# Optimization experiments

Measured on AMD Instinct MI355X. Metric: run time of the kernel, lower is better.

Reference implementation:

```python
import jax, jax.numpy as jnp
import numpy as np

BN_EPS = 1e-5


def setup_inputs() -> dict:
    key = jax.random.key(0)
    k1, k2, k3, k4 = jax.random.split(key, 4)
    B, C, H, W = 16, 128, 128, 128
    x = jax.random.normal(k1, (B, C, H, W), dtype=jnp.float32)
    gamma = jax.random.normal(k2, (1,), dtype=jnp.float32)
    bn_weight = jax.random.uniform(k3, (C,), dtype=jnp.float32)
    bn_bias = jax.random.normal(k4, (C,), dtype=jnp.float32)
    return {"x": x, "gamma": gamma, "bn_weight": bn_weight, "bn_bias": bn_bias}


def reference(x, gamma, bn_weight, bn_bias):
    B, C, H, W = x.shape
    q = x.reshape(B, C, H * W)                      # proj_query: [B, C, HW]
    # energy[b, i, j] = <channel i, channel j>
    energy = jnp.einsum('bin,bjn->bij', q, q)       # [B, C, C]
    energy_new = jnp.max(energy, axis=-1, keepdims=True) - energy
    attention = jax.nn.softmax(energy_new, axis=-1)  # [B, C, C]
    out = jnp.einsum('bij,bjn->bin', attention, q)  # [B, C, HW]
    out = out.reshape(B, C, H, W)
    out = gamma * out
    # BatchNorm2d in training mode: batch statistics over (B, H, W) per channel
    mean = jnp.mean(out, axis=(0, 2, 3), keepdims=True)
    var = jnp.var(out, axis=(0, 2, 3), keepdims=True)  # biased variance
    out = (out - mean) * jax.lax.rsqrt(var + BN_EPS)
    out = out * bn_weight[None, :, None, None] + bn_bias[None, :, None, None]
    return out + x
```

## Files before the change

kernel.cpp:

```cpp
#include <hip/hip_runtime.h>

#define BB 16
#define CC 128
#define NN 16384
#define BN_EPS 1e-5f

typedef unsigned short u16;
typedef short short8 __attribute__((ext_vector_type(8)));
typedef float floatx4 __attribute__((ext_vector_type(4)));

__device__ inline float b2f(u16 u) {
    union { unsigned int i; float f; } c; c.i = ((unsigned int)u) << 16; return c.f;
}
__device__ inline u16 f2b(float f) {
    union { float f; unsigned int i; } c; c.f = f;
    unsigned int r = c.i + 0x7fffu + ((c.i >> 16) & 1u);
    return (u16)(r >> 16);
}

#define K1_LD 72
__global__ __launch_bounds__(256, 4) void k_gram(const float* __restrict__ x,
                                                 float* __restrict__ energy,
                                                 float* __restrict__ S)
{
    __shared__ u16 th[128 * K1_LD];
    __shared__ u16 tl[128 * K1_LD];
    const int b     = blockIdx.x >> 6;
    const int chunk = blockIdx.x & 63;
    const int k0    = chunk * 256;
    const int t     = threadIdx.x;
    const int w = t >> 6, lane = t & 63, quad = lane >> 4, colL = lane & 15;

    floatx4 acc[2][8];
#pragma unroll
    for (int rt = 0; rt < 2; ++rt)
#pragma unroll
        for (int ct = 0; ct < 8; ++ct) acc[rt][ct] = {0.f, 0.f, 0.f, 0.f};
    float rs[8];
#pragma unroll
    for (int it = 0; it < 8; ++it) rs[it] = 0.f;

    const float* xb = x + (size_t)b * CC * NN;
    const int rrow = t >> 4;
    const int c4   = t & 15;
    for (int s = 0; s < 4; ++s) {
        const int ks = k0 + s * 64;
        __syncthreads();
#pragma unroll
        for (int it = 0; it < 8; ++it) {
            int row = it * 16 + rrow;
            float4 v = *(const float4*)(xb + (size_t)row * NN + ks + c4 * 4);
            u16 h0 = f2b(v.x), h1 = f2b(v.y), h2 = f2b(v.z), h3 = f2b(v.w);
            uint2 hv, lv;
            hv.x = (unsigned)h0 | ((unsigned)h1 << 16);
            hv.y = (unsigned)h2 | ((unsigned)h3 << 16);
            lv.x = (unsigned)f2b(v.x - b2f(h0)) | ((unsigned)f2b(v.y - b2f(h1)) << 16);
            lv.y = (unsigned)f2b(v.z - b2f(h2)) | ((unsigned)f2b(v.w - b2f(h3)) << 16);
            *(uint2*)&th[row * K1_LD + c4 * 4] = hv;
            *(uint2*)&tl[row * K1_LD + c4 * 4] = lv;
            rs[it] += (v.x + v.y) + (v.z + v.w);
        }
        __syncthreads();
        const int rbase = w * 32;
#pragma unroll
        for (int ks2 = 0; ks2 < 2; ++ks2) {
            const int kk = ks2 * 32 + quad * 8;
            short8 a0h = *(const short8*)&th[(rbase + colL) * K1_LD + kk];
            short8 a1h = *(const short8*)&th[(rbase + 16 + colL) * K1_LD + kk];
            short8 a0l = *(const short8*)&tl[(rbase + colL) * K1_LD + kk];
            short8 a1l = *(const short8*)&tl[(rbase + 16 + colL) * K1_LD + kk];
#pragma unroll
            for (int ct = 0; ct < 8; ++ct) {
                short8 bh = *(const short8*)&th[(ct * 16 + colL) * K1_LD + kk];
                short8 bl = *(const short8*)&tl[(ct * 16 + colL) * K1_LD + kk];
                acc[0][ct] = __builtin_amdgcn_mfma_f32_16x16x32_bf16(a0h, bh, acc[0][ct], 0, 0, 0);
                acc[1][ct] = __builtin_amdgcn_mfma_f32_16x16x32_bf16(a1h, bh, acc[1][ct], 0, 0, 0);
                acc[0][ct] = __builtin_amdgcn_mfma_f32_16x16x32_bf16(a0l, bh, acc[0][ct], 0, 0, 0);
                acc[1][ct] = __builtin_amdgcn_mfma_f32_16x16x32_bf16(a1l, bh, acc[1][ct], 0, 0, 0);
                acc[0][ct] = __builtin_amdgcn_mfma_f32_16x16x32_bf16(a0h, bl, acc[0][ct], 0, 0, 0);
                acc[1][ct] = __builtin_amdgcn_mfma_f32_16x16x32_bf16(a1h, bl, acc[1][ct], 0, 0, 0);
            }
        }
    }
    float* eb = energy + b * CC * CC;
#pragma unroll
    for (int rt = 0; rt < 2; ++rt)
#pragma unroll
        for (int ct = 0; ct < 8; ++ct)
#pragma unroll
            for (int r = 0; r < 4; ++r) {
                int row = w * 32 + rt * 16 + quad * 4 + r;
                int col = ct * 16 + colL;
                atomicAdd(&eb[row * CC + col], acc[rt][ct][r]);
            }
#pragma unroll
    for (int it = 0; it < 8; ++it) {
        float ps = rs[it];
#pragma unroll
        for (int off = 8; off > 0; off >>= 1) ps += __shfl_down(ps, off, 16);
        if (colL == 0) atomicAdd(&S[b * CC + it * 16 + w * 4 + quad], ps);
    }
}

__global__ __launch_bounds__(256) void k_soft(const float* __restrict__ energy,
                                              const float* __restrict__ S,
                                              u16* __restrict__ attb,
                                              float* __restrict__ meanacc,
                                              float* __restrict__ e2acc)
{
    const int b = blockIdx.x >> 7;
    const int i = blockIdx.x & 127;
    const int t = threadIdx.x;
    __shared__ float att[128];
    __shared__ float red[256];
    const float* E = energy + b * CC * CC;

    float e = (t < 128) ? E[i * CC + t] : 3.0e38f;
    red[t] = e; __syncthreads();
    for (int s2 = 128; s2 > 0; s2 >>= 1) { if (t < s2) red[t] = fminf(red[t], red[t + s2]); __syncthreads(); }
    float emin = red[0]; __syncthreads();

    float a = (t < 128) ? expf(emin - e) : 0.f;
    red[t] = a; __syncthreads();
    for (int s2 = 128; s2 > 0; s2 >>= 1) { if (t < s2) red[t] += red[t + s2]; __syncthreads(); }
    float Z = red[0]; __syncthreads();

    float attf = 0.f;
    if (t < 128) {
        u16 ab = f2b(a / Z);
        attf = b2f(ab);
        attb[((size_t)b * CC + i) * CC + t] = ab;
        att[t] = attf;
    }
    float mp = (t < 128) ? attf * S[b * CC + t] : 0.f;
    red[t] = mp; __syncthreads();
    for (int s2 = 128; s2 > 0; s2 >>= 1) { if (t < s2) red[t] += red[t + s2]; __syncthreads(); }
    if (t == 0) atomicAdd(&meanacc[i], red[0]);
    __syncthreads();

    const int j    = t & 127;
    const int half = t >> 7;
    const float* Ej = E + j * CC + half * 64;
    float inner = 0.f;
#pragma unroll 8
    for (int k = 0; k < 64; ++k) inner += att[half * 64 + k] * Ej[k];
    red[t] = inner; __syncthreads();
    float contrib = (t < 128) ? (red[t] + red[t + 128]) * att[t] : 0.f;
    __syncthreads();
    red[t] = contrib; __syncthreads();
    for (int s2 = 128; s2 > 0; s2 >>= 1) { if (t < s2) red[t] += red[t + s2]; __syncthreads(); }
    if (t == 0) atomicAdd(&e2acc[i], red[0]);
}

#define K3_LD 136
__global__ __launch_bounds__(256, 4) void k_out(const float* __restrict__ x,
                                                const u16* __restrict__ attb,
                                                const float* __restrict__ meanacc,
                                                const float* __restrict__ e2acc,
                                                const float* __restrict__ gamma,
                                                const float* __restrict__ bnw,
                                                const float* __restrict__ bnb,
                                                float* __restrict__ out)
{
    __shared__ u16 qT[128 * K3_LD];
    __shared__ float alpha[128];
    __shared__ float beta[128];
    const int b   = blockIdx.x >> 7;
    const int nn0 = (blockIdx.x & 127) * 128;
    const int t   = threadIdx.x;

    if (t < 128) {
        float g   = gamma[0];
        const float invBN = 1.f / (float)(BB * NN);
        float m   = g * meanacc[t] * invBN;
        float e2  = g * g * e2acc[t] * invBN;
        float var = e2 - m * m;
        float inv = rsqrtf(var + BN_EPS);
        float wv  = bnw[t];
        alpha[t] = g * wv * inv;
        beta[t]  = bnb[t] - m * wv * inv;
    }

    const float* xb = x + (size_t)b * CC * NN + nn0;
    const int n0 = (t & 31) * 4;
#pragma unroll
    for (int rep = 0; rep < 4; ++rep) {
        const int c0 = ((t >> 5) + rep * 8) * 4;
        float4 f0 = *(const float4*)(xb + (size_t)(c0 + 0) * NN + n0);
        float4 f1 = *(const float4*)(xb + (size_t)(c0 + 1) * NN + n0);
        float4 f2 = *(const float4*)(xb + (size_t)(c0 + 2) * NN + n0);
        float4 f3 = *(const float4*)(xb + (size_t)(c0 + 3) * NN + n0);
        const float fx[4] = {f0.x, f1.x, f2.x, f3.x};
        const float fy[4] = {f0.y, f1.y, f2.y, f3.y};
        const float fz[4] = {f0.z, f1.z, f2.z, f3.z};
        const float fw[4] = {f0.w, f1.w, f2.w, f3.w};
        const float* cols[4] = {fx, fy, fz, fw};
#pragma unroll
        for (int jn = 0; jn < 4; ++jn) {
            int n = n0 + jn;
            int g = ((c0 >> 3) + n) & 15;
            uint2 v;
            v.x = (unsigned)f2b(cols[jn][0]) | ((unsigned)f2b(cols[jn][1]) << 16);
            v.y = (unsigned)f2b(cols[jn][2]) | ((unsigned)f2b(cols[jn][3]) << 16);
            *(uint2*)&qT[n * K3_LD + g * 8 + (c0 & 7)] = v;
        }
    }
    __syncthreads();

    const int w = t >> 6, lane = t & 63, quad = lane >> 4, colL = lane & 15;
    const u16* ag = attb + (size_t)b * CC * CC;
    floatx4 acc[8][2];
#pragma unroll
    for (int rt = 0; rt < 8; ++rt) { acc[rt][0] = {0.f,0.f,0.f,0.f}; acc[rt][1] = {0.f,0.f,0.f,0.f}; }

#pragma unroll
    for (int ks = 0; ks < 4; ++ks) {
        const int kk = ks * 32 + quad * 8;
        const int n_a = w * 32 + colL;
        const int n_b = n_a + 16;
        short8 bf0 = *(const short8*)&qT[n_a * K3_LD + ((((kk) >> 3) + n_a) & 15) * 8];
        short8 bf1 = *(const short8*)&qT[n_b * K3_LD + ((((kk) >> 3) + n_b) & 15) * 8];
#pragma unroll
        for (int rt = 0; rt < 8; ++rt) {
            short8 af = *(const short8*)&ag[(rt * 16 + colL) * CC + kk];
            acc[rt][0] = __builtin_amdgcn_mfma_f32_16x16x32_bf16(af, bf0, acc[rt][0], 0, 0, 0);
            acc[rt][1] = __builtin_amdgcn_mfma_f32_16x16x32_bf16(af, bf1, acc[rt][1], 0, 0, 0);
        }
    }

    float* ob = out + (size_t)b * CC * NN + nn0;
#pragma unroll
    for (int rt = 0; rt < 8; ++rt)
#pragma unroll
        for (int ct = 0; ct < 2; ++ct)
#pragma unroll
            for (int r = 0; r < 4; ++r) {
                int chn = rt * 16 + quad * 4 + r;
                int nn  = w * 32 + ct * 16 + colL;
                float v = alpha[chn] * acc[rt][ct][r] + beta[chn]
                        + xb[(size_t)chn * NN + nn];
                ob[(size_t)chn * NN + nn] = v;
            }
}

extern "C" void kernel_launch(void* const* d_in, const int* in_sizes, int n_in,
                              void* d_out, int out_size, void* d_ws, size_t ws_size,
                              hipStream_t stream)
{
    const float* x     = (const float*)d_in[0];
    const float* gamma = (const float*)d_in[1];
    const float* bnw   = (const float*)d_in[2];
    const float* bnb   = (const float*)d_in[3];
    float* out = (float*)d_out;

    char* ws = (char*)d_ws;
    float* energy  = (float*)(ws);
    float* S       = (float*)(ws + 1048576);
    float* meanacc = (float*)(ws + 1056768);
    float* e2acc   = (float*)(ws + 1057280);
    u16*   attb    = (u16*)(ws + 1057792);

    hipMemsetAsync(ws, 0, 1057792, stream);
    hipLaunchKernelGGL(k_gram, dim3(1024), dim3(256), 0, stream, x, energy, S);
    hipLaunchKernelGGL(k_soft, dim3(2048), dim3(256), 0, stream, energy, S, attb, meanacc, e2acc);
    hipLaunchKernelGGL(k_out,  dim3(2048), dim3(256), 0, stream, x, attb, meanacc, e2acc, gamma, bnw, bnb, out);
}
```

Measured before the change: 368.1 us.

## Split gram rows across block pairs, prefetch next slab, remap blocks by XCD

Reworks the gram kernel so each block covers one half of the output rows over a 512-wide K chunk. The next 64-column slab is prefetched into registers while the current one is converted and multiplied, with explicit barriers between stages. Block indices are also remapped so each batch stays on one XCD for L2 locality. The cost is that every x element is now loaded and split into bf16 twice, once per row-half block, in exchange for latency hiding and fewer accumulator registers.

Measured after the change: 341.0 us. 7.4% less time.

```diff
diff --git a/kernel.cpp b/kernel.cpp
--- a/kernel.cpp
+++ b/kernel.cpp
@@ -25,17 +25,19 @@
 {
     __shared__ u16 th[128 * K1_LD];
     __shared__ u16 tl[128 * K1_LD];
-    const int b     = blockIdx.x >> 6;
-    const int chunk = blockIdx.x & 63;
-    const int k0    = chunk * 256;
-    const int t     = threadIdx.x;
+    const int rbid = blockIdx.x;
+    const int xcd  = rbid & 7;
+    const int li   = rbid >> 3;
+    const int b    = xcd + 8 * (li >> 6);
+    const int sub  = li & 63;
+    const int rowhalf = sub & 1;
+    const int k0   = (sub >> 1) * 512;
+    const int t    = threadIdx.x;
     const int w = t >> 6, lane = t & 63, quad = lane >> 4, colL = lane & 15;
 
-    floatx4 acc[2][8];
-#pragma unroll
-    for (int rt = 0; rt < 2; ++rt)
-#pragma unroll
-        for (int ct = 0; ct < 8; ++ct) acc[rt][ct] = {0.f, 0.f, 0.f, 0.f};
+    floatx4 acc[8];
+#pragma unroll
+    for (int ct = 0; ct < 8; ++ct) acc[ct] = {0.f, 0.f, 0.f, 0.f};
     float rs[8];
 #pragma unroll
     for (int it = 0; it < 8; ++it) rs[it] = 0.f;
@@ -43,62 +45,67 @@
     const float* xb = x + (size_t)b * CC * NN;
     const int rrow = t >> 4;
     const int c4   = t & 15;
-    for (int s = 0; s < 4; ++s) {
-        const int ks = k0 + s * 64;
-        __syncthreads();
+
+    float4 v[8];
+#pragma unroll
+    for (int it = 0; it < 8; ++it)
+        v[it] = *(const float4*)(xb + (size_t)(it * 16 + rrow) * NN + k0 + c4 * 4);
+
+    const int arow = rowhalf * 64 + w * 16 + colL;
+    for (int s = 0; s < 8; ++s) {
 #pragma unroll
         for (int it = 0; it < 8; ++it) {
-            int row = it * 16 + rrow;
-            float4 v = *(const float4*)(xb + (size_t)row * NN + ks + c4 * 4);
-            u16 h0 = f2b(v.x), h1 = f2b(v.y), h2 = f2b(v.z), h3 = f2b(v.w);
+            const int row = it * 16 + rrow;
+            float4 vv = v[it];
+            if (s < 7)
+                v[it] = *(const float4*)(xb + (size_t)row * NN + k0 + (s + 1) * 64 + c4 * 4);
+            u16 h0 = f2b(vv.x), h1 = f2b(vv.y), h2 = f2b(vv.z), h3 = f2b(vv.w);
             uint2 hv, lv;
             hv.x = (unsigned)h0 | ((unsigned)h1 << 16);
             hv.y = (unsigned)h2 | ((unsigned)h3 << 16);
-            lv.x = (unsigned)f2b(v.x - b2f(h0)) | ((unsigned)f2b(v.y - b2f(h1)) << 16);
-            lv.y = (unsigned)f2b(v.z - b2f(h2)) | ((unsigned)f2b(v.w - b2f(h3)) << 16);
+            lv.x = (unsigned)f2b(vv.x - b2f(h0)) | ((unsigned)f2b(vv.y - b2f(h1)) << 16);
+            lv.y = (unsigned)f2b(vv.z - b2f(h2)) | ((unsigned)f2b(vv.w - b2f(h3)) << 16);
             *(uint2*)&th[row * K1_LD + c4 * 4] = hv;
             *(uint2*)&tl[row * K1_LD + c4 * 4] = lv;
-            rs[it] += (v.x + v.y) + (v.z + v.w);
-        }
-        __syncthreads();
-        const int rbase = w * 32;
+            rs[it] += (vv.x + vv.y) + (vv.z + vv.w);
+        }
+        asm volatile("s_waitcnt lgkmcnt(0)" ::: "memory");
+        __builtin_amdgcn_s_barrier();
+
 #pragma unroll
         for (int ks2 = 0; ks2 < 2; ++ks2) {
             const int kk = ks2 * 32 + quad * 8;
-            short8 a0h = *(const short8*)&th[(rbase + colL) * K1_LD + kk];
-            short8 a1h = *(const short8*)&th[(rbase + 16 + colL) * K1_LD + kk];
-            short8 a0l = *(const short8*)&tl[(rbase + colL) * K1_LD + kk];
-            short8 a1l = *(const short8*)&tl[(rbase + 16 + colL) * K1_LD + kk];
+            short8 ah = *(const short8*)&th[arow * K1_LD + kk];
+            short8 al = *(const short8*)&tl[arow * K1_LD + kk];
 #pragma unroll
             for (int ct = 0; ct < 8; ++ct) {
                 short8 bh = *(const short8*)&th[(ct * 16 + colL) * K1_LD + kk];
                 short8 bl = *(const short8*)&tl[(ct * 16 + colL) * K1_LD + kk];
-                acc[0][ct] = __builtin_amdgcn_mfma_f32_16x16x32_bf16(a0h, bh, acc[0][ct], 0, 0, 0);
-                acc[1][ct] = __builtin_amdgcn_mfma_f32_16x16x32_bf16(a1h, bh, acc[1][ct], 0, 0, 0);
-                acc[0][ct] = __builtin_amdgcn_mfma_f32_16x16x32_bf16(a0l, bh, acc[0][ct], 0, 0, 0);
-                acc[1][ct] = __builtin_amdgcn_mfma_f32_16x16x32_bf16(a1l, bh, acc[1][ct], 0, 0, 0);
-                acc[0][ct] = __builtin_amdgcn_mfma_f32_16x16x32_bf16(a0h, bl, acc[0][ct], 0, 0, 0);
-                acc[1][ct] = __builtin_amdgcn_mfma_f32_16x16x32_bf16(a1h, bl, acc[1][ct], 0, 0, 0);
+                acc[ct] = __builtin_amdgcn_mfma_f32_16x16x32_bf16(ah, bh, acc[ct], 0, 0, 0);
+                acc[ct] = __builtin_amdgcn_mfma_f32_16x16x32_bf16(al, bh, acc[ct], 0, 0, 0);
+                acc[ct] = __builtin_amdgcn_mfma_f32_16x16x32_bf16(ah, bl, acc[ct], 0, 0, 0);
             }
         }
-    }
+        asm volatile("s_waitcnt lgkmcnt(0)" ::: "memory");
+        __builtin_amdgcn_s_barrier();
+    }
+
     float* eb = energy + b * CC * CC;
-#pragma unroll
-    for (int rt = 0; rt < 2; ++rt)
-#pragma unroll
-        for (int ct = 0; ct < 8; ++ct)
-#pragma unroll
-            for (int r = 0; r < 4; ++r) {
-                int row = w * 32 + rt * 16 + quad * 4 + r;
-                int col = ct * 16 + colL;
-                atomicAdd(&eb[row * CC + col], acc[rt][ct][r]);
-            }
-#pragma unroll
-    for (int it = 0; it < 8; ++it) {
-        float ps = rs[it];
-#pragma unroll
-        for (int off = 8; off > 0; off >>= 1) ps += __shfl_down(ps, off, 16);
-        if (colL == 0) atomicAdd(&S[b * CC + it * 16 + w * 4 + quad], ps);
+    const int erow = rowhalf * 64 + w * 16 + quad * 4;
+#pragma unroll
+    for (int ct = 0; ct < 8; ++ct)
+#pragma unroll
+        for (int r = 0; r < 4; ++r)
+            atomicAdd(&eb[(erow + r) * CC + ct * 16 + colL], acc[ct][r]);
+
+    if (rowhalf == 0) {
+#pragma unroll
+        for (int it = 0; it < 8; ++it) {
+            float ps = rs[it];
+#pragma unroll
+            for (int off = 8; off > 0; off >>= 1) ps += __shfl_down(ps, off, 16);
+            if (colL == 0) atomicAdd(&S[b * CC + it * 16 + w * 4 + quad], ps);
+        }
     }
 }
 
```
